# Optimization experiments

Measured on AMD Instinct MI355X. Metric: run time of the kernel, lower is better.

Reference implementation:

```python
import jax, jax.numpy as jnp
import numpy as np

DIM = 1024
NUM_HEADS = 16
HEAD_DIM = DIM // NUM_HEADS
ROPE_BASE = 10000.0


def apply_rope(x, pos):
    """x: [B, H, N, D] float32, pos: [B, N] int -> rotated x (rotate-half convention)."""
    d = x.shape[-1]
    # inv_freq: [D/2]
    inv_freq = 1.0 / (ROPE_BASE ** (jnp.arange(0, d, 2, dtype=jnp.float32) / d))
    # angles: [B, 1, N, D/2]
    ang = pos.astype(jnp.float32)[:, None, :, None] * inv_freq
    cos = jnp.concatenate([jnp.cos(ang), jnp.cos(ang)], axis=-1)
    sin = jnp.concatenate([jnp.sin(ang), jnp.sin(ang)], axis=-1)
    x1, x2 = x[..., : d // 2], x[..., d // 2 :]
    rotated = jnp.concatenate([-x2, x1], axis=-1)
    return x * cos + rotated * sin


def setup_inputs() -> dict:
    key = jax.random.key(0)
    ks = jax.random.split(key, 10)
    B, Nq, Nk, C = 4, 512, 2048, DIM
    scale = 0.02
    inp = {
        "query": jax.random.normal(ks[0], (B, Nq, C), dtype=jnp.float32),
        "key": jax.random.normal(ks[1], (B, Nk, C), dtype=jnp.float32),
        "value": jax.random.normal(ks[2], (B, Nk, C), dtype=jnp.float32),
        "qpos": jnp.sort(jax.random.randint(ks[3], (B, Nq), 0, Nk, dtype=jnp.int32), axis=-1),
        "kpos": jnp.sort(jax.random.randint(ks[4], (B, Nk), 0, Nk, dtype=jnp.int32), axis=-1),
        # learned params (qkv_bias=False; output proj has bias, per nn.Linear default)
        "Wq": jax.random.normal(ks[5], (C, C), dtype=jnp.float32) * scale,
        "Wk": jax.random.normal(ks[6], (C, C), dtype=jnp.float32) * scale,
        "Wv": jax.random.normal(ks[7], (C, C), dtype=jnp.float32) * scale,
        "Wp": jax.random.normal(ks[8], (C, C), dtype=jnp.float32) * scale,
        "bp": jax.random.normal(ks[9], (C,), dtype=jnp.float32) * scale,
    }
    return inp


def reference(query, key, value, qpos, kpos, Wq, Wk, Wv, Wp, bp):
    B, Nq, C = query.shape
    Nk = key.shape[1]
    H, D = NUM_HEADS, C // NUM_HEADS
    scale = D ** (-0.5)

    # separate Q/K/V linear projections (bias=False), split heads -> [B, H, N, D]
    q = (query @ Wq.T).reshape(B, Nq, H, D).transpose(0, 2, 1, 3)
    k = (key @ Wk.T).reshape(B, Nk, H, D).transpose(0, 2, 1, 3)
    v = (value @ Wv.T).reshape(B, Nk, H, D).transpose(0, 2, 1, 3)

    # RoPE applied in fp32 (matches the cast-to-float/rotate/cast-back sequence)
    q = apply_rope(q.astype(jnp.float32), qpos).astype(query.dtype)
    k = apply_rope(k.astype(jnp.float32), kpos).astype(key.dtype)

    # scaled dot-product attention (dropout_p = 0.0, non-causal)
    scores = jnp.einsum("bhqd,bhkd->bhqk", q, k) * scale
    attn = jax.nn.softmax(scores, axis=-1)
    x = jnp.einsum("bhqk,bhkd->bhqd", attn, v)

    # merge heads and output projection (with bias)
    x = x.transpose(0, 2, 1, 3).reshape(B, Nq, C)
    x = x @ Wp.T + bp
    return x
```

## Files before the change

kernel.cpp:

```cpp
#include <hip/hip_runtime.h>
#include <math.h>

#define B_ 4
#define NQ 512
#define NK 2048
#define C_ 1024
#define H_ 16
#define D_ 64
#define KK 1024

typedef __attribute__((ext_vector_type(8))) _Float16 half8;
typedef __attribute__((ext_vector_type(4))) _Float16 half4;
typedef __attribute__((ext_vector_type(4))) float float4v;

__device__ __forceinline__ void g2l16(const _Float16* g, _Float16* l)
{
    __builtin_amdgcn_global_load_lds(
        (const __attribute__((address_space(1))) unsigned int*)g,
        (__attribute__((address_space(3))) unsigned int*)l, 16, 0, 0);
}

__global__ __launch_bounds__(256) void cvt_all(const float* __restrict__ W0,
                                               const float* __restrict__ W1,
                                               const float* __restrict__ W2,
                                               const float* __restrict__ W3,
                                               const float* __restrict__ q,
                                               const float* __restrict__ k,
                                               const float* __restrict__ v,
                                               _Float16* __restrict__ W16,
                                               _Float16* __restrict__ xq,
                                               _Float16* __restrict__ xk,
                                               _Float16* __restrict__ xv,
                                               float2* __restrict__ tab)
{
    const int blk = blockIdx.x;
    if (blk >= 22528) {
        const int idx = (blk - 22528) * 256 + threadIdx.x;
        const int p = idx >> 5, i = idx & 31;
        double f = 1.0;
        if (i & 1)  f *= 0.7498942093324559;
        if (i & 2)  f *= 0.5623413251903491;
        if (i & 4)  f *= 0.31622776601683794;
        if (i & 8)  f *= 0.1;
        if (i & 16) f *= 0.01;
        const double ang = (double)p * f;
        const double TWO_PI = 6.2831853071795864769;
        const double INV_TWO_PI = 0.15915494309189533577;
        const float red = (float)(ang - TWO_PI * floor(ang * INV_TWO_PI));
        float s, c;
        sincosf(red, &s, &c);
        tab[idx] = make_float2(c, s);
        return;
    }
    const float* src; _Float16* dst; int row;
    if (blk < 4096) {
        const int w = blk >> 10; row = blk & 1023;
        src = (w == 0) ? W0 : (w == 1) ? W1 : (w == 2) ? W2 : W3;
        dst = W16 + ((size_t)w << 20);
    } else {
        const int b2 = blk - 4096;
        if (b2 < 2048)       { src = q; dst = xq; row = b2; }
        else if (b2 < 10240) { src = k; dst = xk; row = b2 - 2048; }
        else                 { src = v; dst = xv; row = b2 - 10240; }
    }
    const int col = threadIdx.x * 4;
    float4 f = *(const float4*)(src + (size_t)row * 1024 + col);
    half4 h;
    h[0] = (_Float16)f.x; h[1] = (_Float16)f.y;
    h[2] = (_Float16)f.z; h[3] = (_Float16)f.w;
    *(half4*)(dst + (size_t)row * 1024 + col) = h;
}

__device__ __forceinline__ void gemm_body(const _Float16* __restrict__ A,
                                          const _Float16* __restrict__ Bw,
                                          _Float16* __restrict__ Yh,
                                          float* __restrict__ Yf,
                                          int mode, int nsh, int m0, int n0,
                                          const float* __restrict__ bias,
                                          _Float16* sA, _Float16* sB)
{
    const int tid = threadIdx.x;
    const int lane = tid & 63, wave = tid >> 6;
    const int wm = (wave >> 1) * 64, wn = (wave & 1) * 64;
    const int fm = lane & 15, quad = lane >> 4;

    const int srow = wave * 32 + (lane >> 3);
    const int soct = (lane & 7) ^ (srow & 7);
    const _Float16* gA = A  + (size_t)(m0 + srow) * KK + soct * 8;
    const _Float16* gB = Bw + (size_t)(n0 + srow) * KK + soct * 8;

    float4v acc[4][4];
    #pragma unroll
    for (int i = 0; i < 4; ++i)
        #pragma unroll
        for (int j = 0; j < 4; ++j)
            #pragma unroll
            for (int e = 0; e < 4; ++e) acc[i][j][e] = 0.0f;

    for (int k0 = 0; k0 < KK; k0 += 64) {
        __syncthreads();
        #pragma unroll
        for (int u = 0; u < 4; ++u) {
            g2l16(gA + (size_t)u * 8 * KK + k0, &sA[(wave * 32 + u * 8) * 64]);
            g2l16(gB + (size_t)u * 8 * KK + k0, &sB[(wave * 32 + u * 8) * 64]);
        }
        __syncthreads();

        #pragma unroll
        for (int ks = 0; ks < 2; ++ks) {
            const int po = ((ks * 4 + quad) ^ (fm & 7)) * 8;
            half8 a[4], b[4];
            #pragma unroll
            for (int i = 0; i < 4; ++i) {
                a[i] = *(const half8*)&sA[(wm + i * 16 + fm) * 64 + po];
                b[i] = *(const half8*)&sB[(wn + i * 16 + fm) * 64 + po];
            }
            __builtin_amdgcn_s_setprio(1);
            #pragma unroll
            for (int i = 0; i < 4; ++i)
                #pragma unroll
                for (int j = 0; j < 4; ++j)
                    acc[i][j] = __builtin_amdgcn_mfma_f32_16x16x32_f16(a[i], b[j], acc[i][j], 0, 0, 0);
            __builtin_amdgcn_s_setprio(0);
        }
    }

    const int rr = quad * 4;
    if (mode == 0) {
        const int nmask = (1 << nsh) - 1;
        #pragma unroll
        for (int i = 0; i < 4; ++i)
            #pragma unroll
            for (int r = 0; r < 4; ++r) {
                const int m = m0 + wm + i * 16 + rr + r;
                const int b = m >> nsh, n = m & nmask;
                #pragma unroll
                for (int j = 0; j < 4; ++j) {
                    const int c = n0 + wn + j * 16 + fm;
                    Yh[((((size_t)b * H_ + (c >> 6)) << nsh) + n) * 64 + (c & 63)] = (_Float16)acc[i][j][r];
                }
            }
    } else if (mode == 2) {
        const int nmask = (1 << nsh) - 1;
        #pragma unroll
        for (int i = 0; i < 4; ++i)
            #pragma unroll
            for (int r = 0; r < 4; ++r) {
                const int m = m0 + wm + i * 16 + rr + r;
                const int b = m >> nsh, n = m & nmask;
                #pragma unroll
                for (int j = 0; j < 4; ++j) {
                    const int c = n0 + wn + j * 16 + fm;
                    Yh[(((size_t)(b * H_ + (c >> 6)) * 64) + (c & 63)) * NK + n] = (_Float16)acc[i][j][r];
                }
            }
    } else {
        #pragma unroll
        for (int i = 0; i < 4; ++i)
            #pragma unroll
            for (int r = 0; r < 4; ++r) {
                const int m = m0 + wm + i * 16 + rr + r;
                #pragma unroll
                for (int j = 0; j < 4; ++j) {
                    const int c = n0 + wn + j * 16 + fm;
                    Yf[(size_t)m * 1024 + c] = acc[i][j][r] + bias[c];
                }
            }
    }
}

__global__ __launch_bounds__(256) void gemm_qkv(const _Float16* __restrict__ xq,
                                                const _Float16* __restrict__ xk,
                                                const _Float16* __restrict__ xv,
                                                const _Float16* __restrict__ W16,
                                                _Float16* __restrict__ qhp,
                                                _Float16* __restrict__ khp,
                                                _Float16* __restrict__ vtp)
{
    __shared__ _Float16 sA[128 * 64];
    __shared__ _Float16 sB[128 * 64];

    const int lbid = blockIdx.x;
    const int xcd = lbid & 7;
    const int seq = lbid >> 3;
    const int y = xcd + 8 * (seq >> 3);
    const int n0 = (seq & 7) * 128;

    if (y < 64)
        gemm_body(xk, W16 + (1u << 20), khp, nullptr, 0, 11, y * 128, n0, nullptr, sA, sB);
    else if (y < 128)
        gemm_body(xv, W16 + (2u << 20), vtp, nullptr, 2, 11, (y - 64) * 128, n0, nullptr, sA, sB);
    else
        gemm_body(xq, W16, qhp, nullptr, 0, 9, (y - 128) * 128, n0, nullptr, sA, sB);
}

__global__ __launch_bounds__(256) void gemm_out(const _Float16* __restrict__ A,
                                                const _Float16* __restrict__ Bw,
                                                float* __restrict__ Yf,
                                                const float* __restrict__ bias)
{
    __shared__ _Float16 sA[128 * 64];
    __shared__ _Float16 sB[128 * 64];
    gemm_body(A, Bw, nullptr, Yf, 1, 0, blockIdx.y * 128, blockIdx.x * 128, bias, sA, sB);
}

__global__ __launch_bounds__(256) void rope_tab(_Float16* __restrict__ qh,
                                                _Float16* __restrict__ kh,
                                                const int* __restrict__ qpos,
                                                const int* __restrict__ kpos,
                                                const float2* __restrict__ tab)
{
    const int idx = blockIdx.x * 256 + threadIdx.x;
    const int row = idx >> 3;
    const int d0 = (idx & 7) * 4;

    _Float16* ptr; int p; float scale;
    if (row < 32768) {
        ptr = qh + (size_t)row * 64;
        p = qpos[(row >> 13) * 512 + (row & 511)];
        scale = 0.125f;
    } else {
        const int rk = row - 32768;
        ptr = kh + (size_t)rk * 64;
        p = kpos[(rk >> 15) * 2048 + (rk & 2047)];
        scale = 1.0f;
    }

    half4 x1 = *(const half4*)(ptr + d0);
    half4 x2 = *(const half4*)(ptr + d0 + 32);
    const float2* tb = tab + p * 32 + d0;
    half4 o1, o2;
    #pragma unroll
    for (int u = 0; u < 4; ++u) {
        const float2 cs = tb[u];
        const float a = (float)x1[u], b = (float)x2[u];
        o1[u] = (_Float16)((a * cs.x - b * cs.y) * scale);
        o2[u] = (_Float16)((b * cs.x + a * cs.y) * scale);
    }
    *(half4*)(ptr + d0)      = o1;
    *(half4*)(ptr + d0 + 32) = o2;
}

__global__ __launch_bounds__(512) void attn_fused(const _Float16* __restrict__ qh,
                                                  const _Float16* __restrict__ kh,
                                                  const _Float16* __restrict__ vt,
                                                  _Float16* __restrict__ xw16)
{
    __shared__ _Float16 sK[2][64 * 64];
    __shared__ _Float16 sV[2][64 * 64];
    __shared__ _Float16 ps[8][16][66];

    const int tid = threadIdx.x;
    const int lane = tid & 63, wv = tid >> 6;
    const int bhi = blockIdx.x & 63;
    const int qquad = blockIdx.x >> 6;
    const size_t bh = (size_t)bhi;
    const int qt = qquad * 8 + wv;

    const int fm = lane & 15;
    const int quad = lane >> 4;
    const int fq = quad * 8;

    const _Float16* kb = kh + bh * NK * 64;
    const _Float16* vb = vt + bh * (size_t)64 * NK;

    const int r0 = lane >> 3;
    const int c4 = lane & 7;
    const int sch = c4 ^ r0;
    const _Float16* gK = kb + (size_t)(wv * 8 + r0) * 64 + sch * 8;
    const _Float16* gV = vb + (size_t)(wv * 8 + r0) * NK + sch * 8;

    const _Float16* qb = qh + (bh * NQ + (size_t)qt * 16) * 64;
    half8 aq[2];
    aq[0] = *(const half8*)(qb + (size_t)fm * 64 + fq);
    aq[1] = *(const half8*)(qb + (size_t)fm * 64 + 32 + fq);

    float l_acc[4] = {};
    float4v O[4];
    #pragma unroll
    for (int j = 0; j < 4; ++j)
        #pragma unroll
        for (int e = 0; e < 4; ++e) O[j][e] = 0.0f;

    const float4v z4 = {0.0f, 0.0f, 0.0f, 0.0f};

    g2l16(gK, &sK[0][wv * 512]);
    g2l16(gV, &sV[0][wv * 512]);
    __syncthreads();

    for (int it = 0; it < 32; ++it) {
        const int cur = it & 1;
        if (it < 31) {
            g2l16(gK + (size_t)(it + 1) * 64 * 64, &sK[cur ^ 1][wv * 512]);
            g2l16(gV + (it + 1) * 64,              &sV[cur ^ 1][wv * 512]);
        }
        const _Float16* Kc = sK[cur];
        const _Float16* Vc = sV[cur];

        half8 bk[4][2];
        #pragma unroll
        for (int j = 0; j < 4; ++j)
            #pragma unroll
            for (int ks = 0; ks < 2; ++ks)
                bk[j][ks] = *(const half8*)&Kc[(j * 16 + fm) * 64 + (((ks * 4 + quad) ^ (fm & 7)) * 8)];

        float4v s[4];
        __builtin_amdgcn_s_setprio(1);
        #pragma unroll
        for (int j = 0; j < 4; ++j) {
            s[j] = __builtin_amdgcn_mfma_f32_16x16x32_f16(aq[0], bk[j][0], z4, 0, 0, 0);
            s[j] = __builtin_amdgcn_mfma_f32_16x16x32_f16(aq[1], bk[j][1], s[j], 0, 0, 0);
        }
        __builtin_amdgcn_s_setprio(0);

        half8 bv[4][2];
        #pragma unroll
        for (int j = 0; j < 4; ++j)
            #pragma unroll
            for (int ks = 0; ks < 2; ++ks)
                bv[j][ks] = *(const half8*)&Vc[(j * 16 + fm) * 64 + (((ks * 4 + quad) ^ (fm & 7)) * 8)];

        #pragma unroll
        for (int j = 0; j < 4; ++j)
            #pragma unroll
            for (int r = 0; r < 4; ++r) {
                const float p = __expf(s[j][r]);
                l_acc[r] += p;
                ps[wv][quad * 4 + r][16 * j + fm] = (_Float16)p;
            }

        __builtin_amdgcn_s_setprio(1);
        #pragma unroll
        for (int ks = 0; ks < 2; ++ks) {
            half8 pa = *(const half8*)&ps[wv][fm][ks * 32 + fq];
            #pragma unroll
            for (int j = 0; j < 4; ++j)
                O[j] = __builtin_amdgcn_mfma_f32_16x16x32_f16(pa, bv[j][ks], O[j], 0, 0, 0);
        }
        __builtin_amdgcn_s_setprio(0);

        __syncthreads();
    }

    #pragma unroll
    for (int r = 0; r < 4; ++r) {
        float l = l_acc[r];
        l += __shfl_xor(l, 1);
        l += __shfl_xor(l, 2);
        l += __shfl_xor(l, 4);
        l += __shfl_xor(l, 8);
        const float inv = 1.0f / l;
        const int qr = quad * 4 + r;
        const int row = (bhi >> 4) * 512 + qt * 16 + qr;
        #pragma unroll
        for (int j = 0; j < 4; ++j) {
            const int col = (bhi & 15) * 64 + j * 16 + fm;
            xw16[(size_t)row * 1024 + col] = (_Float16)(O[j][r] * inv);
        }
    }
}

extern "C" void kernel_launch(void* const* d_in, const int* in_sizes, int n_in,
                              void* d_out, int out_size, void* d_ws, size_t ws_size,
                              hipStream_t stream)
{
    const float* query = (const float*)d_in[0];
    const float* key   = (const float*)d_in[1];
    const float* value = (const float*)d_in[2];
    const int*   qpos  = (const int*)d_in[3];
    const int*   kpos  = (const int*)d_in[4];
    const float* Wq    = (const float*)d_in[5];
    const float* Wk    = (const float*)d_in[6];
    const float* Wv    = (const float*)d_in[7];
    const float* Wp    = (const float*)d_in[8];
    const float* bp    = (const float*)d_in[9];
    float* out = (float*)d_out;

    char* ws = (char*)d_ws;
    _Float16* xk16  = (_Float16*)(ws);
    _Float16* xv16  = (_Float16*)(ws + (16u << 20));
    _Float16* xq16  = (_Float16*)(ws + (32u << 20));
    _Float16* W16   = (_Float16*)(ws + (36u << 20));
    _Float16* qhp   = (_Float16*)(ws + (44u << 20));
    _Float16* khp   = (_Float16*)(ws + (48u << 20));
    _Float16* vtp   = (_Float16*)(ws + (64u << 20));
    float2*   tab   = (float2*)d_out;

    cvt_all<<<22784, 256, 0, stream>>>(Wq, Wk, Wv, Wp, query, key, value,
                                       W16, xq16, xk16, xv16, tab);

    gemm_qkv<<<1152, 256, 0, stream>>>(xq16, xk16, xv16, W16, qhp, khp, vtp);

    rope_tab<<<5120, 256, 0, stream>>>(qhp, khp, qpos, kpos, tab);

    attn_fused<<<256, 512, 0, stream>>>(qhp, khp, vtp, xq16);

    gemm_out<<<dim3(8, 16), 256, 0, stream>>>(xq16, W16 + (3u << 20), out, bp);
}
```

Baseline: 256.5 us.

## Triple-buffer K/V tiles in attention with 4-wave blocks and explicit vmcnt waits

The attention kernel now launches 512 blocks of 256 threads (4 waves, each owning a 16-row query tile) instead of 256 blocks of 512. K/V tiles are staged in a three-deep LDS ring, prefetching two tiles ahead. Hand-placed s_waitcnt vmcnt and raw s_barrier replace __syncthreads so loads stay in flight across iterations. Each wave issues twice as many async loads per tile, and correctness depends on the hard-coded vmcnt counts matching the number of outstanding loads.

```diff
diff --git a/kernel.cpp b/kernel.cpp
--- a/kernel.cpp
+++ b/kernel.cpp
@@ -241,21 +241,21 @@
     *(half4*)(ptr + d0 + 32) = o2;
 }
 
-__global__ __launch_bounds__(512) void attn_fused(const _Float16* __restrict__ qh,
+__global__ __launch_bounds__(256) void attn_fused(const _Float16* __restrict__ qh,
                                                   const _Float16* __restrict__ kh,
                                                   const _Float16* __restrict__ vt,
                                                   _Float16* __restrict__ xw16)
 {
-    __shared__ _Float16 sK[2][64 * 64];
-    __shared__ _Float16 sV[2][64 * 64];
-    __shared__ _Float16 ps[8][16][66];
+    __shared__ _Float16 sK[3][64 * 64];
+    __shared__ _Float16 sV[3][64 * 64];
+    __shared__ _Float16 ps[4][16][66];
 
     const int tid = threadIdx.x;
     const int lane = tid & 63, wv = tid >> 6;
     const int bhi = blockIdx.x & 63;
-    const int qquad = blockIdx.x >> 6;
+    const int qoct = blockIdx.x >> 6;
     const size_t bh = (size_t)bhi;
-    const int qt = qquad * 8 + wv;
+    const int qt = qoct * 4 + wv;
 
     const int fm = lane & 15;
     const int quad = lane >> 4;
@@ -267,8 +267,15 @@
     const int r0 = lane >> 3;
     const int c4 = lane & 7;
     const int sch = c4 ^ r0;
-    const _Float16* gK = kb + (size_t)(wv * 8 + r0) * 64 + sch * 8;
-    const _Float16* gV = vb + (size_t)(wv * 8 + r0) * NK + sch * 8;
+    const _Float16* gK = kb + (size_t)(wv * 16 + r0) * 64 + sch * 8;
+    const _Float16* gV = vb + (size_t)(wv * 16 + r0) * NK + sch * 8;
+
+#define STAGE(bf, t) do {                                                     \
+        g2l16(gK + (size_t)(t) * 4096,        &sK[bf][(wv * 16) * 64]);       \
+        g2l16(gK + (size_t)(t) * 4096 + 512,  &sK[bf][(wv * 16 + 8) * 64]);   \
+        g2l16(gV + (t) * 64,                  &sV[bf][(wv * 16) * 64]);       \
+        g2l16(gV + (size_t)8 * NK + (t) * 64, &sV[bf][(wv * 16 + 8) * 64]);   \
+    } while (0)
 
     const _Float16* qb = qh + (bh * NQ + (size_t)qt * 16) * 64;
     half8 aq[2];
@@ -284,16 +291,21 @@
 
     const float4v z4 = {0.0f, 0.0f, 0.0f, 0.0f};
 
-    g2l16(gK, &sK[0][wv * 512]);
-    g2l16(gV, &sV[0][wv * 512]);
-    __syncthreads();
+    STAGE(0, 0);
+    STAGE(1, 1);
 
     for (int it = 0; it < 32; ++it) {
-        const int cur = it & 1;
-        if (it < 31) {
-            g2l16(gK + (size_t)(it + 1) * 64 * 64, &sK[cur ^ 1][wv * 512]);
-            g2l16(gV + (it + 1) * 64,              &sV[cur ^ 1][wv * 512]);
-        }
+        const int cur = it % 3;
+        if (it + 2 < 32)
+            STAGE((it + 2) % 3, it + 2);
+
+        if (it < 30)       asm volatile("s_waitcnt vmcnt(8)" ::: "memory");
+        else if (it == 30) asm volatile("s_waitcnt vmcnt(4)" ::: "memory");
+        else               asm volatile("s_waitcnt vmcnt(0)" ::: "memory");
+        __builtin_amdgcn_sched_barrier(0);
+        __builtin_amdgcn_s_barrier();
+        __builtin_amdgcn_sched_barrier(0);
+
         const _Float16* Kc = sK[cur];
         const _Float16* Vc = sV[cur];
 
@@ -339,8 +351,12 @@
         }
         __builtin_amdgcn_s_setprio(0);
 
-        __syncthreads();
-    }
+        asm volatile("s_waitcnt lgkmcnt(0)" ::: "memory");
+        __builtin_amdgcn_sched_barrier(0);
+        __builtin_amdgcn_s_barrier();
+        __builtin_amdgcn_sched_barrier(0);
+    }
+#undef STAGE
 
     #pragma unroll
     for (int r = 0; r < 4; ++r) {
@@ -393,7 +409,7 @@
 
     rope_tab<<<5120, 256, 0, stream>>>(qhp, khp, qpos, kpos, tab);
 
-    attn_fused<<<256, 512, 0, stream>>>(qhp, khp, vtp, xq16);
+    attn_fused<<<512, 256, 0, stream>>>(qhp, khp, vtp, xq16);
 
     gemm_out<<<dim3(8, 16), 256, 0, stream>>>(xq16, W16 + (3u << 20), out, bp);
 }
```

New measurement: 245.0 us. 4.5% less time.
